# Optimization experiments

Measured on AMD Instinct MI355X. Metric: run time of the kernel, lower is better.

## Reference

```python
import jax, jax.numpy as jnp
import numpy as np

B, S, H, U = 32, 4096, 512, 512


def setup_inputs() -> dict:
    key = jax.random.key(0)
    ks = jax.random.split(key, 6)
    scale = 1.0 / np.sqrt(H)
    return {
        "query": jax.random.normal(ks[0], (B, H), dtype=jnp.float32),
        "values": jax.random.normal(ks[1], (B, S, H), dtype=jnp.float32),
        "W1": jax.random.normal(ks[2], (H, U), dtype=jnp.float32) * scale,
        "b1": jnp.zeros((U,), dtype=jnp.float32),
        "W2": jax.random.normal(ks[3], (H, U), dtype=jnp.float32) * scale,
        "b2": jnp.zeros((U,), dtype=jnp.float32),
        "va": jax.random.normal(ks[4], (U, 1), dtype=jnp.float32) * (1.0 / np.sqrt(U)),
        "bva": jnp.zeros((1,), dtype=jnp.float32),
    }


def reference(query, values, W1, b1, W2, b2, va, bva):
    # query: [B, H] -> [B, 1, U]; values: [B, S, H] -> [B, S, U]
    q_proj = jnp.einsum('bh,hu->bu', query, W1) + b1           # [B, U]
    v_proj = jnp.einsum('bsh,hu->bsu', values, W2) + b2        # [B, S, U]
    scores = jnp.einsum('bsu,uo->bso', jnp.tanh(q_proj[:, None, :] + v_proj), va) + bva  # [B, S, 1]
    attention_weights = jax.nn.softmax(scores, axis=1)         # [B, S, 1]
    context_vector = jnp.sum(attention_weights * values, axis=1)  # [B, H]
    return attention_weights, context_vector
```

## Files before the change

kernel.cpp:

```cpp
#include <hip/hip_runtime.h>
#include <stdint.h>

#define B_SZ 32
#define S_SZ 4096
#define H_SZ 512
#define U_SZ 512

typedef __attribute__((ext_vector_type(8))) _Float16 half8;
typedef __attribute__((ext_vector_type(4))) float floatx4;

__device__ __forceinline__ void async_copy16(const void* g, void* l) {
    __builtin_amdgcn_global_load_lds(
        (const __attribute__((address_space(1))) void*)g,
        (__attribute__((address_space(3))) void*)l, 16, 0, 0);
}

__global__ __launch_bounds__(256) void prep_kernel(
    const float* __restrict__ W2, const float* __restrict__ b1,
    const float* __restrict__ b2, const float* __restrict__ bva,
    const float* __restrict__ query, const float* __restrict__ W1,
    _Float16* __restrict__ W2s, float* __restrict__ qpb2,
    float* __restrict__ scores, float* __restrict__ ctx)
{
    const int t = threadIdx.x;
    const int rb = blockIdx.x;
    if (rb < 1024) {
        const int i = rb * 256 + t;
        const int k = i >> 9, n = i & 511;
        W2s[(k >> 5) * 16384 + ((k >> 3) & 3) * 4096 + n * 8 + (k & 7)] =
            (_Float16)W2[i];
    } else if (rb < 1536) {
        scores[(rb - 1024) * 256 + t] = *bva;
    } else if (rb < 1600) {
        ctx[(rb - 1536) * 256 + t] = 0.0f;
    } else {
        const int bq = rb - 1600;
        const int b = bq >> 1, uc = bq & 1;
        const int u = uc * 256 + t;
        const float* q  = query + b * H_SZ;
        const float* Wp = W1 + u;
        float a0 = 0.f, a1 = 0.f, a2 = 0.f, a3 = 0.f;
        for (int k = 0; k < 512; k += 4) {
            a0 = fmaf(q[k],     Wp[(size_t)k * U_SZ],       a0);
            a1 = fmaf(q[k + 1], Wp[(size_t)(k + 1) * U_SZ], a1);
            a2 = fmaf(q[k + 2], Wp[(size_t)(k + 2) * U_SZ], a2);
            a3 = fmaf(q[k + 3], Wp[(size_t)(k + 3) * U_SZ], a3);
        }
        qpb2[b * U_SZ + u] = (a0 + a1) + (a2 + a3) + b1[u] + b2[u];
    }
}

__global__ __launch_bounds__(256, 4) void scores_kernel(
    const float* __restrict__ A, const _Float16* __restrict__ W2s,
    const float* __restrict__ qpb2, const float* __restrict__ va,
    float* __restrict__ scores)
{
    __shared__ __align__(16) float    Albs[2][4096];
    __shared__ __align__(16) _Float16 Blbs[2][4096];
    __shared__ float red[256];

    const int t  = threadIdx.x;
    const int w  = t >> 6, l = t & 63;
    const int c  = l & 15, g4 = l >> 4;
    const int mh = w >> 1, nh = w & 1;
    const int bidx = (int)blockIdx.x;
    const int lb   = (bidx & 7) * 512 + (bidx >> 3);
    const int n0 = (lb & 3) * 128;
    const int m0 = (lb >> 2) * 128;
    const int b  = m0 >> 12;

    floatx4 acc[4][4];
#pragma unroll
    for (int mt = 0; mt < 4; ++mt)
#pragma unroll
        for (int nt = 0; nt < 4; ++nt) acc[mt][nt] = (floatx4)(0.0f);

    const float*    Ab0 = A + (size_t)m0 * H_SZ;
    const _Float16* Wb0 = W2s + n0 * 8;

    auto stage = [&](int kb, int buf) {
        const float* Vb = Ab0 + kb * 32;
#pragma unroll
        for (int i = 0; i < 4; ++i) {
            const int j = t + i * 256;
            const int g = j >> 7, ml = j & 127;
            async_copy16(Vb + (size_t)ml * H_SZ + g * 4, &Albs[buf][j * 4]);
        }
        const _Float16* Wb = Wb0 + kb * 16384;
#pragma unroll
        for (int i = 0; i < 2; ++i) {
            const int j = t + i * 256;
            const int kq = j >> 7, nl = j & 127;
            async_copy16(Wb + kq * 4096 + nl * 8, &Blbs[buf][j * 8]);
        }
    };

    stage(0, 0);
    __syncthreads();

    for (int kb = 0; kb < 16; ++kb) {
        const int cur = kb & 1;
        if (kb < 15) stage(kb + 1, cur ^ 1);
        half8 af[4];
#pragma unroll
        for (int mt = 0; mt < 4; ++mt) {
            const int ml = mh * 64 + mt * 16 + c;
            float4 lo = *(const float4*)&Albs[cur][((2 * g4)     * 128 + ml) * 4];
            float4 hi = *(const float4*)&Albs[cur][((2 * g4 + 1) * 128 + ml) * 4];
            half8 a;
            a[0] = (_Float16)lo.x; a[1] = (_Float16)lo.y;
            a[2] = (_Float16)lo.z; a[3] = (_Float16)lo.w;
            a[4] = (_Float16)hi.x; a[5] = (_Float16)hi.y;
            a[6] = (_Float16)hi.z; a[7] = (_Float16)hi.w;
            af[mt] = a;
        }
        half8 bf[4];
#pragma unroll
        for (int nt = 0; nt < 4; ++nt) {
            const int nl = nh * 64 + nt * 16 + c;
            bf[nt] = *(const half8*)&Blbs[cur][(g4 * 128 + nl) * 8];
        }
#pragma unroll
        for (int mt = 0; mt < 4; ++mt)
#pragma unroll
            for (int nt = 0; nt < 4; ++nt)
                acc[mt][nt] = __builtin_amdgcn_mfma_f32_16x16x32_f16(
                    af[mt], bf[nt], acc[mt][nt], 0, 0, 0);
        __syncthreads();
    }

    float qv2[4], vv[4], vv2[4];
#pragma unroll
    for (int nt = 0; nt < 4; ++nt) {
        const int n = n0 + nh * 64 + nt * 16 + c;
        const float q = qpb2[b * U_SZ + n];
        const float v = va[n];
        qv2[nt] = 2.0f * q;
        vv[nt] = v;
        vv2[nt] = 2.0f * v;
    }
#pragma unroll
    for (int mt = 0; mt < 4; ++mt) {
#pragma unroll
        for (int r = 0; r < 4; ++r) {
            float p = 0.0f;
#pragma unroll
            for (int nt = 0; nt < 4; ++nt) {
                const float ex = __expf(fmaf(acc[mt][nt][r], 2.0f, qv2[nt]));
                const float rc = __builtin_amdgcn_rcpf(ex + 1.0f);
                p = fmaf(-vv2[nt], rc, p + vv[nt]);
            }
            p += __shfl_xor(p, 1);
            p += __shfl_xor(p, 2);
            p += __shfl_xor(p, 4);
            p += __shfl_xor(p, 8);
            if (c == 0)
                red[(mh * 64 + mt * 16 + g4 * 4 + r) * 2 + nh] = p;
        }
    }
    __syncthreads();
    if (t < 128)
        atomicAdd(&scores[m0 + t], red[t * 2] + red[t * 2 + 1]);
}

__global__ __launch_bounds__(1024) void sredux_kernel(
    const float* __restrict__ scores, float* __restrict__ ML)
{
    __shared__ float red[16];
    __shared__ float s_max;
    const int b = blockIdx.x;
    const int t = threadIdx.x;
    float4 v = *(const float4*)(scores + b * S_SZ + t * 4);
    float m = fmaxf(fmaxf(v.x, v.y), fmaxf(v.z, v.w));
#pragma unroll
    for (int o = 32; o > 0; o >>= 1) m = fmaxf(m, __shfl_xor(m, o));
    if ((t & 63) == 0) red[t >> 6] = m;
    __syncthreads();
    if (t == 0) {
        float mm = red[0];
        for (int i = 1; i < 16; ++i) mm = fmaxf(mm, red[i]);
        s_max = mm;
    }
    __syncthreads();
    const float mm = s_max;
    float s = __expf(v.x - mm) + __expf(v.y - mm) +
              __expf(v.z - mm) + __expf(v.w - mm);
#pragma unroll
    for (int o = 32; o > 0; o >>= 1) s += __shfl_xor(s, o);
    if ((t & 63) == 0) red[t >> 6] = s;
    __syncthreads();
    if (t == 0) {
        float ss = 0.0f;
        for (int i = 0; i < 16; ++i) ss += red[i];
        ML[b * 2] = mm;
        ML[b * 2 + 1] = ss;
    }
}

__global__ __launch_bounds__(256) void context_f32_kernel(
    const float* __restrict__ values, const float* __restrict__ scores,
    const float* __restrict__ ML, float* __restrict__ out)
{
    __shared__ float wl[128];
    __shared__ __align__(16) float part[4][512];
    const int sc = blockIdx.x, b = blockIdx.y;
    const int t = threadIdx.x;
    const int s0 = sc * 128;
    const float M = ML[b * 2];
    const float rL = 1.0f / ML[b * 2 + 1];
    if (t < 32) {
        float4 sv = *(const float4*)(scores + b * S_SZ + s0 + t * 4);
        float4 wv;
        wv.x = __expf(sv.x - M) * rL; wv.y = __expf(sv.y - M) * rL;
        wv.z = __expf(sv.z - M) * rL; wv.w = __expf(sv.w - M) * rL;
        *(float4*)&wl[t * 4] = wv;
        *(float4*)(out + b * S_SZ + s0 + t * 4) = wv;
    }
    __syncthreads();

    const int g = t >> 6, l = t & 63;
    const float* vp = values + ((size_t)b * S_SZ + s0 + g * 32) * H_SZ + l * 4;
    float4 a00 = {0,0,0,0}, a01 = {0,0,0,0}, a10 = {0,0,0,0}, a11 = {0,0,0,0};
    for (int i = 0; i < 32; i += 2) {
        const float w0 = wl[g * 32 + i];
        const float w1 = wl[g * 32 + i + 1];
        const float* r0 = vp + (size_t)i * H_SZ;
        const float* r1 = r0 + H_SZ;
        float4 v00 = *(const float4*)(r0);
        float4 v01 = *(const float4*)(r0 + 256);
        float4 v10 = *(const float4*)(r1);
        float4 v11 = *(const float4*)(r1 + 256);
        a00.x = fmaf(w0, v00.x, a00.x); a00.y = fmaf(w0, v00.y, a00.y);
        a00.z = fmaf(w0, v00.z, a00.z); a00.w = fmaf(w0, v00.w, a00.w);
        a01.x = fmaf(w0, v01.x, a01.x); a01.y = fmaf(w0, v01.y, a01.y);
        a01.z = fmaf(w0, v01.z, a01.z); a01.w = fmaf(w0, v01.w, a01.w);
        a10.x = fmaf(w1, v10.x, a10.x); a10.y = fmaf(w1, v10.y, a10.y);
        a10.z = fmaf(w1, v10.z, a10.z); a10.w = fmaf(w1, v10.w, a10.w);
        a11.x = fmaf(w1, v11.x, a11.x); a11.y = fmaf(w1, v11.y, a11.y);
        a11.z = fmaf(w1, v11.z, a11.z); a11.w = fmaf(w1, v11.w, a11.w);
    }
    a00.x += a10.x; a00.y += a10.y; a00.z += a10.z; a00.w += a10.w;
    a01.x += a11.x; a01.y += a11.y; a01.z += a11.z; a01.w += a11.w;
    *(float4*)&part[g][l * 4] = a00;
    *(float4*)&part[g][256 + l * 4] = a01;
    __syncthreads();

    float* ctx = out + B_SZ * S_SZ;
#pragma unroll
    for (int rep = 0; rep < 2; ++rep) {
        const int h = rep * 256 + t;
        const float s = (part[0][h] + part[1][h]) + (part[2][h] + part[3][h]);
        atomicAdd(&ctx[b * H_SZ + h], s);
    }
}

extern "C" void kernel_launch(void* const* d_in, const int* in_sizes, int n_in,
                              void* d_out, int out_size, void* d_ws, size_t ws_size,
                              hipStream_t stream) {
    const float* query  = (const float*)d_in[0];
    const float* values = (const float*)d_in[1];
    const float* W1     = (const float*)d_in[2];
    const float* b1     = (const float*)d_in[3];
    const float* W2     = (const float*)d_in[4];
    const float* b2     = (const float*)d_in[5];
    const float* va     = (const float*)d_in[6];
    const float* bva    = (const float*)d_in[7];
    float* out = (float*)d_out;

    char* ws = (char*)d_ws;
    float*    qpb2   = (float*)ws;
    _Float16* W2s    = (_Float16*)(ws + 65536);
    float*    scores = (float*)(ws + 589824);
    float*    ML     = (float*)(ws + 1114112);

    float* ctx = out + B_SZ * S_SZ;

    prep_kernel<<<1664, 256, 0, stream>>>(
        W2, b1, b2, bva, query, W1, W2s, qpb2, scores, ctx);
    scores_kernel<<<4096, 256, 0, stream>>>(values, W2s, qpb2, va, scores);
    sredux_kernel<<<32, 1024, 0, stream>>>(scores, ML);
    context_f32_kernel<<<dim3(32, 32), 256, 0, stream>>>(values, scores, ML, out);
}
```

Measured before the change: 586.1 us.

## Stage A tile through registers, converting to fp16 once before LDS store

```diff
diff --git a/kernel.cpp b/kernel.cpp
--- a/kernel.cpp
+++ b/kernel.cpp
@@ -55,7 +55,7 @@
     const float* __restrict__ qpb2, const float* __restrict__ va,
     float* __restrict__ scores)
 {
-    __shared__ __align__(16) float    Albs[2][4096];
+    __shared__ __align__(16) _Float16 Albs[2][4096];
     __shared__ __align__(16) _Float16 Blbs[2][4096];
     __shared__ float red[256];
 
@@ -75,17 +75,33 @@
 #pragma unroll
         for (int nt = 0; nt < 4; ++nt) acc[mt][nt] = (floatx4)(0.0f);
 
-    const float*    Ab0 = A + (size_t)m0 * H_SZ;
-    const _Float16* Wb0 = W2s + n0 * 8;
-
-    auto stage = [&](int kb, int buf) {
-        const float* Vb = Ab0 + kb * 32;
-#pragma unroll
-        for (int i = 0; i < 4; ++i) {
-            const int j = t + i * 256;
-            const int g = j >> 7, ml = j & 127;
-            async_copy16(Vb + (size_t)ml * H_SZ + g * 4, &Albs[buf][j * 4]);
-        }
+    const int ml = t & 127;
+    const int ga = t >> 7;
+    const float*    Arow = A + (size_t)(m0 + ml) * H_SZ;
+    const _Float16* Wb0  = W2s + n0 * 8;
+
+    float4 ra0, ra1, ra2, ra3;
+    auto loadA = [&](int kb) {
+        const float* p = Arow + kb * 32 + ga * 8;
+        ra0 = *(const float4*)(p);
+        ra1 = *(const float4*)(p + 4);
+        ra2 = *(const float4*)(p + 16);
+        ra3 = *(const float4*)(p + 20);
+    };
+    auto cvtwrite = [&](int buf) {
+        half8 h0, h1;
+        h0[0] = (_Float16)ra0.x; h0[1] = (_Float16)ra0.y;
+        h0[2] = (_Float16)ra0.z; h0[3] = (_Float16)ra0.w;
+        h0[4] = (_Float16)ra1.x; h0[5] = (_Float16)ra1.y;
+        h0[6] = (_Float16)ra1.z; h0[7] = (_Float16)ra1.w;
+        h1[0] = (_Float16)ra2.x; h1[1] = (_Float16)ra2.y;
+        h1[2] = (_Float16)ra2.z; h1[3] = (_Float16)ra2.w;
+        h1[4] = (_Float16)ra3.x; h1[5] = (_Float16)ra3.y;
+        h1[6] = (_Float16)ra3.z; h1[7] = (_Float16)ra3.w;
+        *(half8*)&Albs[buf][(ga * 128 + ml) * 8]       = h0;
+        *(half8*)&Albs[buf][((ga + 2) * 128 + ml) * 8] = h1;
+    };
+    auto stageB = [&](int kb, int buf) {
         const _Float16* Wb = Wb0 + kb * 16384;
 #pragma unroll
         for (int i = 0; i < 2; ++i) {
@@ -95,24 +111,22 @@
         }
     };
 
-    stage(0, 0);
+    stageB(0, 0);
+    loadA(0);
+    cvtwrite(0);
     __syncthreads();
 
     for (int kb = 0; kb < 16; ++kb) {
         const int cur = kb & 1;
-        if (kb < 15) stage(kb + 1, cur ^ 1);
+        if (kb < 15) {
+            loadA(kb + 1);
+            stageB(kb + 1, cur ^ 1);
+        }
         half8 af[4];
 #pragma unroll
         for (int mt = 0; mt < 4; ++mt) {
-            const int ml = mh * 64 + mt * 16 + c;
-            float4 lo = *(const float4*)&Albs[cur][((2 * g4)     * 128 + ml) * 4];
-            float4 hi = *(const float4*)&Albs[cur][((2 * g4 + 1) * 128 + ml) * 4];
-            half8 a;
-            a[0] = (_Float16)lo.x; a[1] = (_Float16)lo.y;
-            a[2] = (_Float16)lo.z; a[3] = (_Float16)lo.w;
-            a[4] = (_Float16)hi.x; a[5] = (_Float16)hi.y;
-            a[6] = (_Float16)hi.z; a[7] = (_Float16)hi.w;
-            af[mt] = a;
+            const int mll = mh * 64 + mt * 16 + c;
+            af[mt] = *(const half8*)&Albs[cur][(g4 * 128 + mll) * 8];
         }
         half8 bf[4];
 #pragma unroll
@@ -126,6 +140,7 @@
             for (int nt = 0; nt < 4; ++nt)
                 acc[mt][nt] = __builtin_amdgcn_mfma_f32_16x16x32_f16(
                     af[mt], bf[nt], acc[mt][nt], 0, 0, 0);
+        if (kb < 15) cvtwrite(cur ^ 1);
         __syncthreads();
     }
 
```

Measured after the change: 543.2 us. -7.3%, faster.
